# Optimization experiments

Measured on AMD Instinct MI355X. Metric: run time of the kernel, lower is better.

## Reference

```python
import jax, jax.numpy as jnp
import numpy as np

IN_DIM = 100000   # entity vocab
H_DIM = 128       # h_dim == dist_dim (forced in __init__)
K = 16            # num_neighbor
BOUNDARIES = jnp.array([1.0, 2.0, 4.0, 8.0, 16.0, 32.0, 64.0, 128.0], dtype=jnp.float32)
N_BUCKETS = BOUNDARIES.shape[0] + 1


def setup_inputs() -> dict:
    key = jax.random.key(0)
    ks = jax.random.split(key, 8)
    N = 100000
    node_ids = jax.random.randint(ks[0], (N,), 0, IN_DIM)
    nbr_idx = jax.random.randint(ks[1], (N, K), 0, N)
    nbr_dist = jax.random.uniform(ks[2], (N, K), dtype=jnp.float32) * 200.0
    scale = 1.0 / np.sqrt(H_DIM)
    embed_table = jax.random.normal(ks[3], (IN_DIM, H_DIM), dtype=jnp.float32) * scale
    dist_table = jax.random.normal(ks[4], (N_BUCKETS, H_DIM), dtype=jnp.float32) * scale
    W_self = jax.random.normal(ks[5], (H_DIM, H_DIM), dtype=jnp.float32) * scale
    W_nbr = jax.random.normal(ks[6], (H_DIM, H_DIM), dtype=jnp.float32) * scale
    b = jnp.zeros((H_DIM,), dtype=jnp.float32)
    return {
        "node_ids": node_ids, "nbr_idx": nbr_idx, "nbr_dist": nbr_dist,
        "embed_table": embed_table, "dist_table": dist_table,
        "W_self": W_self, "W_nbr": W_nbr, "b": b,
    }


def reference(node_ids, nbr_idx, nbr_dist, embed_table, dist_table, W_self, W_nbr, b):
    # h = self.embedding(h.squeeze())
    h = embed_table[node_ids]                       # [N, D] gather
    # DistRelConv: gather sampled neighbor features
    neigh = h[nbr_idx]                              # [N, K, D] gather
    # bucketize edge distances against boundaries -> distance-bucket embedding
    bucket = jnp.searchsorted(BOUNDARIES, nbr_dist) # [N, K] int
    msg = neigh + dist_table[bucket]                # [N, K, D]
    agg = jnp.mean(msg, axis=1)                     # [N, D]
    # merge='sum': self transform + neighbor transform, relu activation
    out = jax.nn.relu(h @ W_self + agg @ W_nbr + b) # [N, D]
    return out
```

## Files before the change

### kernel.cpp

```cpp
#include <hip/hip_runtime.h>
#include <stdint.h>

#define KNBR 16

typedef float f32x4 __attribute__((ext_vector_type(4)));
typedef float f32x2 __attribute__((ext_vector_type(2)));
typedef __bf16 bf16x8 __attribute__((ext_vector_type(8)));

union ABFrag { uint4 u; bf16x8 v; };

__device__ __forceinline__ uint32_t bf16_rne(float x) {
    uint32_t u = __float_as_uint(x);
    return (u + 0x7fffu + ((u >> 16) & 1u)) >> 16;
}

__device__ __forceinline__ uint32_t bucket_of(float d) {
    uint32_t u = __float_as_uint(d);
    int e = (int)((u >> 23) & 0xff) - 127;
    int b = e + ((u & 0x7fffffu) != 0 ? 1 : 0);
    return (uint32_t)min(max(b, 0), 8);
}

#define GLD(gsrc, ldst)                                                          \
    __builtin_amdgcn_global_load_lds(                                            \
        (const __attribute__((address_space(1))) void*)(gsrc),                   \
        (__attribute__((address_space(3))) void*)(ldst), 4, 0, 0)

__global__ void k_prep(const float* __restrict__ src, uint32_t* __restrict__ ebf,
                       uint32_t* __restrict__ e8, int n_dwords,
                       const float* __restrict__ Ws, const float* __restrict__ Wn,
                       uint16_t* __restrict__ Bp) {
    if (blockIdx.x < 2048) {
        int i = blockIdx.x * blockDim.x + threadIdx.x;
        int stride = 2048 * blockDim.x;
        for (; i < n_dwords; i += stride) {
            float4 v = ((const float4*)src)[i];
            ebf[2 * i]     = bf16_rne(v.x) | (bf16_rne(v.y) << 16);
            ebf[2 * i + 1] = bf16_rne(v.z) | (bf16_rne(v.w) << 16);
            uint32_t p = 0;
            p = __builtin_amdgcn_cvt_pk_fp8_f32(v.x, v.y, p, false);
            p = __builtin_amdgcn_cvt_pk_fp8_f32(v.z, v.w, p, true);
            e8[i] = p;
        }
    } else {
        int o = (blockIdx.x - 2048) * blockDim.x + threadIdx.x;
        if (o >= 8 * 8 * 64 * 8) return;
        int i = o & 7, lane = (o >> 3) & 63, nt = (o >> 9) & 7, ks = o >> 12;
        int r = ks * 32 + (lane >> 4) * 8 + i;
        int c = nt * 16 + (lane & 15);
        float v = (r < 128) ? Ws[r * 128 + c] : Wn[(r - 128) * 128 + c];
        Bp[o] = (uint16_t)bf16_rne(v);
    }
}

__global__ __launch_bounds__(256, 5) void k_fused(
    const int* __restrict__ node_ids, const int* __restrict__ nbr_idx,
    const float* __restrict__ nbr_dist,
    const uint32_t* __restrict__ emb_bf, const uint16_t* __restrict__ emb8,
    const float* __restrict__ dist_table, const float* __restrict__ bias,
    const uint32_t* __restrict__ Bp, float* __restrict__ out, int nht)
{
    __shared__ uint32_t L[4 * 2048];

    const int lane = threadIdx.x & 63;
    const int w = threadIdx.x >> 6;
    const int l_hi = lane >> 4;
    const int l_lo = lane & 15;
    uint32_t* Aw = L + w * 2048;
    uint32_t* Sw = Aw + 1024;
    float* Fw = (float*)Aw;

    const int ht = blockIdx.x * 4 + w;
    if (ht >= nht) return;

    f32x2 dreg[9];
    #pragma unroll
    for (int b = 0; b < 9; ++b) {
        float2 t = *(const float2*)(dist_table + b * 128 + 2 * lane);
        dreg[b] = (f32x2){t.x, t.y};
    }
    float breg[8];
    #pragma unroll
    for (int nt = 0; nt < 8; ++nt) breg[nt] = bias[nt * 16 + l_lo];

    int2 nb = *(const int2*)(nbr_idx + (size_t)ht * 128 + lane * 2);
    float2 dd = *(const float2*)(nbr_dist + (size_t)ht * 128 + lane * 2);
    uint32_t ea[2];
    ea[0] = ((uint32_t)node_ids[nb.x] & 0xFFFFFFu) | (bucket_of(dd.x) << 24);
    ea[1] = ((uint32_t)node_ids[nb.y] & 0xFFFFFFu) | (bucket_of(dd.y) << 24);
    uint32_t selfv = (uint32_t)node_ids[(size_t)ht * 8 + (lane & 7)];


#define ISSUE(J) do {                                                                     \
        const int sw_ = ((J) & 7) << 2;                                                   \
        const uint32_t sid_ = (uint32_t)__builtin_amdgcn_readlane((int)selfv, (J));       \
        GLD(emb_bf + (size_t)sid_ * 64 + (lane ^ sw_), Aw + (J) * 128);                   \
        uint32_t* sb_ = Sw + ((J) & 1) * 512;                                             \
        _Pragma("unroll")                                                                 \
        for (int m = 0; m < 8; ++m) {                                                     \
            const int L_ = 8 * (J) + m;                                                   \
            const uint32_t s0_ = (uint32_t)__builtin_amdgcn_readlane((int)ea[0], L_) & 0xFFFFFFu; \
            const uint32_t s1_ = (uint32_t)__builtin_amdgcn_readlane((int)ea[1], L_) & 0xFFFFFFu; \
            const uint32_t sel_ = (lane < 32) ? s0_ : s1_;                                \
            GLD((const uint8_t*)emb8 + (size_t)sel_ * 128 + (lane & 31) * 4, sb_ + m * 64); \
        }                                                                                 \
    } while (0)

#define CONSUME(J, VM) do {                                                               \
        asm volatile("s_waitcnt vmcnt(" #VM ")" ::: "memory");                            \
        const uint16_t* st_ = (const uint16_t*)(Sw + ((J) & 1) * 512);                    \
        f32x2 s_ = (f32x2){0.f, 0.f};                                                     \
        uint64_t c_ = 0;                                                                  \
        _Pragma("unroll")                                                                 \
        for (int k = 0; k < KNBR; ++k) {                                                  \
            const uint32_t ew_ = (uint32_t)__builtin_amdgcn_readlane((int)ea[k & 1], 8 * (J) + (k >> 1)); \
            c_ += 1ull << (5 * (ew_ >> 24));                                              \
            const uint32_t pv_ = (uint32_t)st_[k * 64 + lane];                            \
            s_ += __builtin_amdgcn_cvt_pk_f32_fp8(pv_, false);                            \
        }                                                                                 \
        _Pragma("unroll")                                                                 \
        for (int b = 0; b < 9; ++b) {                                                     \
            const float fb_ = (float)(uint32_t)((c_ >> (5 * b)) & 31u);                   \
            s_ += (f32x2){fb_, fb_} * dreg[b];                                            \
        }                                                                                 \
        s_ *= 0.0625f;                                                                    \
        const int sw_ = ((J) & 7) << 2;                                                   \
        Aw[(J) * 128 + (64 + (lane ^ sw_))] = bf16_rne(s_.x) | (bf16_rne(s_.y) << 16);    \
        __builtin_amdgcn_sched_barrier(0);                                                \
    } while (0)

    ISSUE(0); ISSUE(1);
    CONSUME(0, 9);  ISSUE(2);
    CONSUME(1, 9);  ISSUE(3);
    CONSUME(2, 9);  ISSUE(4);
    CONSUME(3, 9);  ISSUE(5);
    CONSUME(4, 9);  ISSUE(6);
    CONSUME(5, 9);  ISSUE(7);
    CONSUME(6, 9);
    CONSUME(7, 0);
#undef ISSUE
#undef CONSUME

    asm volatile("s_waitcnt vmcnt(0) lgkmcnt(0)" ::: "memory");
    __builtin_amdgcn_sched_barrier(0);

    f32x4 acc[8];
    #pragma unroll
    for (int t = 0; t < 8; ++t) acc[t] = (f32x4){0.f, 0.f, 0.f, 0.f};
    #pragma unroll
    for (int ks = 0; ks < 8; ++ks) {
        ABFrag a;
        a.u = *(const uint4*)(Aw + l_lo * 128 + ((ks * 16 + l_hi * 4) ^ ((l_lo & 7) << 2)));
        #pragma unroll
        for (int nt = 0; nt < 8; ++nt) {
            ABFrag b;
            b.u = ((const uint4*)Bp)[(ks * 8 + nt) * 64 + lane];
            acc[nt] = __builtin_amdgcn_mfma_f32_16x16x32_bf16(a.v, b.v, acc[nt], 0, 0, 0);
        }
    }

    #pragma unroll
    for (int nt = 0; nt < 8; ++nt) {
        const int col = nt * 16 + l_lo;
        #pragma unroll
        for (int r = 0; r < 4; ++r) {
            const int row = l_hi * 4 + r;
            if (row < 8) {
                float v = acc[nt][r] + breg[nt];
                Fw[row * 128 + (col ^ ((row & 7) << 2))] = v > 0.f ? v : 0.f;
            }
        }
    }
    float* dst = out + (size_t)ht * 1024;
    #pragma unroll
    for (int it = 0; it < 4; ++it) {
        const int f = it * 256 + lane * 4;
        const int r = f >> 7, c = f & 127;
        float4 v = *(const float4*)(Fw + r * 128 + (c ^ ((r & 7) << 2)));
        *(float4*)(dst + f) = v;
    }
}

__global__ void k_naive(const int* __restrict__ node_ids, const int* __restrict__ nbr_idx,
                        const float* __restrict__ nbr_dist, const float* __restrict__ emb,
                        const float* __restrict__ dt, const float* __restrict__ Ws,
                        const float* __restrict__ Wn, const float* __restrict__ bias,
                        float* __restrict__ out, int base) {
    __shared__ float h[128], ag[128];
    const int nd = base + blockIdx.x;
    const int t = threadIdx.x;
    const int nid = node_ids[nd];
    float hv = emb[(size_t)nid * 128 + t];
    float a = 0.f;
    for (int k = 0; k < KNBR; ++k) {
        int sn = node_ids[nbr_idx[(size_t)nd * KNBR + k]];
        int bkt = (int)bucket_of(nbr_dist[(size_t)nd * KNBR + k]);
        a += emb[(size_t)sn * 128 + t] + dt[bkt * 128 + t];
    }
    h[t] = hv; ag[t] = a * 0.0625f;
    __syncthreads();
    float s = bias[t];
    for (int d = 0; d < 128; ++d) s += h[d] * Ws[d * 128 + t] + ag[d] * Wn[d * 128 + t];
    out[(size_t)nd * 128 + t] = s > 0.f ? s : 0.f;
}

extern "C" void kernel_launch(void* const* d_in, const int* in_sizes, int n_in,
                              void* d_out, int out_size, void* d_ws, size_t ws_size,
                              hipStream_t stream) {
    const int* node_ids   = (const int*)d_in[0];
    const int* nbr_idx    = (const int*)d_in[1];
    const float* nbr_dist = (const float*)d_in[2];
    const float* emb      = (const float*)d_in[3];
    const float* dist_tab = (const float*)d_in[4];
    const float* Ws       = (const float*)d_in[5];
    const float* Wn       = (const float*)d_in[6];
    const float* bias     = (const float*)d_in[7];
    float* out = (float*)d_out;
    const int n = in_sizes[0];
    const int in_dim = in_sizes[3] / 128;

    const size_t offEbf = 65536;
    const size_t offE8  = offEbf + (size_t)in_dim * 256;
    const size_t needT  = offE8 + (size_t)in_dim * 128;

    if (ws_size < needT) {
        if (n > 0)
            k_naive<<<n, 128, 0, stream>>>(node_ids, nbr_idx, nbr_dist, emb, dist_tab, Ws, Wn, bias, out, 0);
        return;
    }
    uint16_t* Bp   = (uint16_t*)d_ws;
    uint32_t* ebf  = (uint32_t*)((char*)d_ws + offEbf);
    uint32_t* e8   = (uint32_t*)((char*)d_ws + offE8);

    k_prep<<<2176, 256, 0, stream>>>(emb, ebf, e8, in_dim * 32, Ws, Wn, Bp);

    const int nht = n >> 3;
    const int rem = n & 7;

    if (nht > 0) {
        const int nblocks = (nht + 3) >> 2;
        k_fused<<<nblocks, 256, 0, stream>>>(node_ids, nbr_idx, nbr_dist, ebf, (const uint16_t*)e8,
                                             dist_tab, bias, (const uint32_t*)Bp, out, nht);
    }
    if (rem > 0)
        k_naive<<<rem, 128, 0, stream>>>(node_ids, nbr_idx, nbr_dist, emb, dist_tab, Ws, Wn, bias, out, nht << 3);
}
```

Baseline: 82.76 us.

## Process two 8-node tiles per wave, overlapping next tile's gathers with MFMA

Each wave now handles two consecutive 8-node tiles. It prefetches the second tile's neighbor indices and distances while consuming the first, then issues the second tile's first gathers before running the first tile's MFMA and epilogue. The aim is to hide gather latency behind matrix math and the output store. In exchange, LDS per wave rises by half, launch bounds drop from 5 to 3, and the grid shrinks to half as many blocks, which lowers occupancy and parallelism.

```diff
diff --git a/kernel.cpp b/kernel.cpp
--- a/kernel.cpp
+++ b/kernel.cpp
@@ -53,25 +53,29 @@
     }
 }
 
-__global__ __launch_bounds__(256, 5) void k_fused(
+__global__ __launch_bounds__(256, 3) void k_fused(
     const int* __restrict__ node_ids, const int* __restrict__ nbr_idx,
     const float* __restrict__ nbr_dist,
     const uint32_t* __restrict__ emb_bf, const uint16_t* __restrict__ emb8,
     const float* __restrict__ dist_table, const float* __restrict__ bias,
     const uint32_t* __restrict__ Bp, float* __restrict__ out, int nht)
 {
-    __shared__ uint32_t L[4 * 2048];
+    __shared__ uint32_t L[4 * 3072];
 
     const int lane = threadIdx.x & 63;
     const int w = threadIdx.x >> 6;
     const int l_hi = lane >> 4;
     const int l_lo = lane & 15;
-    uint32_t* Aw = L + w * 2048;
-    uint32_t* Sw = Aw + 1024;
-    float* Fw = (float*)Aw;
-
-    const int ht = blockIdx.x * 4 + w;
-    if (ht >= nht) return;
+    uint32_t* const wbase = L + w * 3072;
+    uint32_t* const A0 = wbase;
+    uint32_t* const A1 = wbase + 1024;
+    uint32_t* const Sw = wbase + 2048;
+
+    const int wid = blockIdx.x * 4 + w;
+    const int ht0 = wid * 2;
+    if (ht0 >= nht) return;
+    const bool has1 = (ht0 + 1 < nht);
+    const int ht1c = min(ht0 + 1, nht - 1);
 
     f32x2 dreg[9];
     #pragma unroll
@@ -83,37 +87,37 @@
     #pragma unroll
     for (int nt = 0; nt < 8; ++nt) breg[nt] = bias[nt * 16 + l_lo];
 
-    int2 nb = *(const int2*)(nbr_idx + (size_t)ht * 128 + lane * 2);
-    float2 dd = *(const float2*)(nbr_dist + (size_t)ht * 128 + lane * 2);
-    uint32_t ea[2];
-    ea[0] = ((uint32_t)node_ids[nb.x] & 0xFFFFFFu) | (bucket_of(dd.x) << 24);
-    ea[1] = ((uint32_t)node_ids[nb.y] & 0xFFFFFFu) | (bucket_of(dd.y) << 24);
-    uint32_t selfv = (uint32_t)node_ids[(size_t)ht * 8 + (lane & 7)];
-
-
-#define ISSUE(J) do {                                                                     \
+    int2 nb = *(const int2*)(nbr_idx + (size_t)ht0 * 128 + lane * 2);
+    float2 dd = *(const float2*)(nbr_dist + (size_t)ht0 * 128 + lane * 2);
+    uint32_t selfv = (uint32_t)node_ids[(size_t)ht0 * 8 + (lane & 7)];
+    uint32_t ea0 = ((uint32_t)node_ids[nb.x] & 0xFFFFFFu) | (bucket_of(dd.x) << 24);
+    uint32_t ea1 = ((uint32_t)node_ids[nb.y] & 0xFFFFFFu) | (bucket_of(dd.y) << 24);
+
+
+#define ISSUE(J, AW) do {                                                                 \
         const int sw_ = ((J) & 7) << 2;                                                   \
         const uint32_t sid_ = (uint32_t)__builtin_amdgcn_readlane((int)selfv, (J));       \
-        GLD(emb_bf + (size_t)sid_ * 64 + (lane ^ sw_), Aw + (J) * 128);                   \
+        GLD(emb_bf + (size_t)sid_ * 64 + (lane ^ sw_), (AW) + (J) * 128);                 \
         uint32_t* sb_ = Sw + ((J) & 1) * 512;                                             \
         _Pragma("unroll")                                                                 \
         for (int m = 0; m < 8; ++m) {                                                     \
             const int L_ = 8 * (J) + m;                                                   \
-            const uint32_t s0_ = (uint32_t)__builtin_amdgcn_readlane((int)ea[0], L_) & 0xFFFFFFu; \
-            const uint32_t s1_ = (uint32_t)__builtin_amdgcn_readlane((int)ea[1], L_) & 0xFFFFFFu; \
+            const uint32_t s0_ = (uint32_t)__builtin_amdgcn_readlane((int)ea0, L_) & 0xFFFFFFu; \
+            const uint32_t s1_ = (uint32_t)__builtin_amdgcn_readlane((int)ea1, L_) & 0xFFFFFFu; \
             const uint32_t sel_ = (lane < 32) ? s0_ : s1_;                                \
             GLD((const uint8_t*)emb8 + (size_t)sel_ * 128 + (lane & 31) * 4, sb_ + m * 64); \
         }                                                                                 \
     } while (0)
 
-#define CONSUME(J, VM) do {                                                               \
+#define CONSUME(J, VM, AW) do {                                                           \
         asm volatile("s_waitcnt vmcnt(" #VM ")" ::: "memory");                            \
         const uint16_t* st_ = (const uint16_t*)(Sw + ((J) & 1) * 512);                    \
         f32x2 s_ = (f32x2){0.f, 0.f};                                                     \
         uint64_t c_ = 0;                                                                  \
         _Pragma("unroll")                                                                 \
         for (int k = 0; k < KNBR; ++k) {                                                  \
-            const uint32_t ew_ = (uint32_t)__builtin_amdgcn_readlane((int)ea[k & 1], 8 * (J) + (k >> 1)); \
+            const uint32_t ew_ = (uint32_t)__builtin_amdgcn_readlane(                     \
+                (int)((k & 1) ? ea1 : ea0), 8 * (J) + (k >> 1));                          \
             c_ += 1ull << (5 * (ew_ >> 24));                                              \
             const uint32_t pv_ = (uint32_t)st_[k * 64 + lane];                            \
             s_ += __builtin_amdgcn_cvt_pk_f32_fp8(pv_, false);                            \
@@ -125,60 +129,100 @@
         }                                                                                 \
         s_ *= 0.0625f;                                                                    \
         const int sw_ = ((J) & 7) << 2;                                                   \
-        Aw[(J) * 128 + (64 + (lane ^ sw_))] = bf16_rne(s_.x) | (bf16_rne(s_.y) << 16);    \
+        (AW)[(J) * 128 + (64 + (lane ^ sw_))] = bf16_rne(s_.x) | (bf16_rne(s_.y) << 16);  \
         __builtin_amdgcn_sched_barrier(0);                                                \
     } while (0)
 
-    ISSUE(0); ISSUE(1);
-    CONSUME(0, 9);  ISSUE(2);
-    CONSUME(1, 9);  ISSUE(3);
-    CONSUME(2, 9);  ISSUE(4);
-    CONSUME(3, 9);  ISSUE(5);
-    CONSUME(4, 9);  ISSUE(6);
-    CONSUME(5, 9);  ISSUE(7);
-    CONSUME(6, 9);
-    CONSUME(7, 0);
+#define MFMA_EPI(AW, HT) do {                                                             \
+        f32x4 acc[8];                                                                     \
+        _Pragma("unroll")                                                                 \
+        for (int t = 0; t < 8; ++t) acc[t] = (f32x4){0.f, 0.f, 0.f, 0.f};                 \
+        _Pragma("unroll")                                                                 \
+        for (int ks = 0; ks < 8; ++ks) {                                                  \
+            ABFrag a;                                                                     \
+            a.u = *(const uint4*)((AW) + l_lo * 128 + ((ks * 16 + l_hi * 4) ^ ((l_lo & 7) << 2))); \
+            _Pragma("unroll")                                                             \
+            for (int nt = 0; nt < 8; ++nt) {                                              \
+                ABFrag b;                                                                 \
+                b.u = ((const uint4*)Bp)[(ks * 8 + nt) * 64 + lane];                      \
+                acc[nt] = __builtin_amdgcn_mfma_f32_16x16x32_bf16(a.v, b.v, acc[nt], 0, 0, 0); \
+            }                                                                             \
+        }                                                                                 \
+        ISSUE_NEXT_HOOK;                                                                  \
+        float* Fw_ = (float*)(AW);                                                       \
+        _Pragma("unroll")                                                                 \
+        for (int nt = 0; nt < 8; ++nt) {                                                  \
+            const int col = nt * 16 + l_lo;                                               \
+            _Pragma("unroll")                                                             \
+            for (int r = 0; r < 4; ++r) {                                                 \
+                const int row = l_hi * 4 + r;                                             \
+                if (row < 8) {                                                            \
+                    float v = acc[nt][r] + breg[nt];                                      \
+                    Fw_[row * 128 + (col ^ ((row & 7) << 2))] = v > 0.f ? v : 0.f;        \
+                }                                                                         \
+            }                                                                             \
+        }                                                                                 \
+        float* dst_ = out + (size_t)(HT) * 1024;                                          \
+        _Pragma("unroll")                                                                 \
+        for (int it = 0; it < 4; ++it) {                                                  \
+            const int f = it * 256 + lane * 4;                                            \
+            const int r = f >> 7, c = f & 127;                                            \
+            float4 v = *(const float4*)(Fw_ + r * 128 + (c ^ ((r & 7) << 2)));            \
+            *(float4*)(dst_ + f) = v;                                                     \
+        }                                                                                 \
+    } while (0)
+
+    ISSUE(0, A0); ISSUE(1, A0);
+
+    CONSUME(0, 9, A0);  ISSUE(2, A0);
+    CONSUME(1, 9, A0);
+    int2 nb2 = *(const int2*)(nbr_idx + (size_t)ht1c * 128 + lane * 2);
+    float2 dd2 = *(const float2*)(nbr_dist + (size_t)ht1c * 128 + lane * 2);
+    uint32_t sv2 = (uint32_t)node_ids[(size_t)ht1c * 8 + (lane & 7)];
+    __builtin_amdgcn_sched_barrier(0);
+    ISSUE(3, A0);
+    CONSUME(2, 12, A0); ISSUE(4, A0);
+    CONSUME(3, 9, A0);  ISSUE(5, A0);
+    CONSUME(4, 9, A0);  ISSUE(6, A0);
+    int nid2x = node_ids[nb2.x];
+    int nid2y = node_ids[nb2.y];
+    __builtin_amdgcn_sched_barrier(0);
+    CONSUME(5, 11, A0); ISSUE(7, A0);
+    CONSUME(6, 11, A0);
+    CONSUME(7, 0, A0);
+
+    const uint32_t ean0 = ((uint32_t)nid2x & 0xFFFFFFu) | (bucket_of(dd2.x) << 24);
+    const uint32_t ean1 = ((uint32_t)nid2y & 0xFFFFFFu) | (bucket_of(dd2.y) << 24);
+
+    asm volatile("s_waitcnt lgkmcnt(0)" ::: "memory");
+    __builtin_amdgcn_sched_barrier(0);
+
+    ea0 = ean0; ea1 = ean1; selfv = sv2;
+#define ISSUE_NEXT_HOOK do { if (has1) { ISSUE(0, A1); ISSUE(1, A1); } } while (0)
+    MFMA_EPI(A0, ht0);
+#undef ISSUE_NEXT_HOOK
+
+    if (!has1) return;
+
+    CONSUME(0, 9, A1);  ISSUE(2, A1);
+    CONSUME(1, 9, A1);  ISSUE(3, A1);
+    CONSUME(2, 9, A1);  ISSUE(4, A1);
+    CONSUME(3, 9, A1);  ISSUE(5, A1);
+    CONSUME(4, 9, A1);  ISSUE(6, A1);
+    CONSUME(5, 9, A1);  ISSUE(7, A1);
+    CONSUME(6, 9, A1);
+    CONSUME(7, 0, A1);
+
+    asm volatile("s_waitcnt lgkmcnt(0)" ::: "memory");
+    __builtin_amdgcn_sched_barrier(0);
+
+#define ISSUE_NEXT_HOOK do { } while (0)
+    MFMA_EPI(A1, ht0 + 1);
+#undef ISSUE_NEXT_HOOK
+
 #undef ISSUE
 #undef CONSUME
-
-    asm volatile("s_waitcnt vmcnt(0) lgkmcnt(0)" ::: "memory");
-    __builtin_amdgcn_sched_barrier(0);
-
-    f32x4 acc[8];
-    #pragma unroll
-    for (int t = 0; t < 8; ++t) acc[t] = (f32x4){0.f, 0.f, 0.f, 0.f};
-    #pragma unroll
-    for (int ks = 0; ks < 8; ++ks) {
-        ABFrag a;
-        a.u = *(const uint4*)(Aw + l_lo * 128 + ((ks * 16 + l_hi * 4) ^ ((l_lo & 7) << 2)));
-        #pragma unroll
-        for (int nt = 0; nt < 8; ++nt) {
-            ABFrag b;
-            b.u = ((const uint4*)Bp)[(ks * 8 + nt) * 64 + lane];
-            acc[nt] = __builtin_amdgcn_mfma_f32_16x16x32_bf16(a.v, b.v, acc[nt], 0, 0, 0);
-        }
-    }
-
-    #pragma unroll
-    for (int nt = 0; nt < 8; ++nt) {
-        const int col = nt * 16 + l_lo;
-        #pragma unroll
-        for (int r = 0; r < 4; ++r) {
-            const int row = l_hi * 4 + r;
-            if (row < 8) {
-                float v = acc[nt][r] + breg[nt];
-                Fw[row * 128 + (col ^ ((row & 7) << 2))] = v > 0.f ? v : 0.f;
-            }
-        }
-    }
-    float* dst = out + (size_t)ht * 1024;
-    #pragma unroll
-    for (int it = 0; it < 4; ++it) {
-        const int f = it * 256 + lane * 4;
-        const int r = f >> 7, c = f & 127;
-        float4 v = *(const float4*)(Fw + r * 128 + (c ^ ((r & 7) << 2)));
-        *(float4*)(dst + f) = v;
-    }
+#undef MFMA_EPI
 }
 
 __global__ void k_naive(const int* __restrict__ node_ids, const int* __restrict__ nbr_idx,
@@ -238,7 +282,7 @@
     const int rem = n & 7;
 
     if (nht > 0) {
-        const int nblocks = (nht + 3) >> 2;
+        const int nblocks = (nht + 7) >> 3;
         k_fused<<<nblocks, 256, 0, stream>>>(node_ids, nbr_idx, nbr_dist, ebf, (const uint16_t*)e8,
                                              dist_tab, bias, (const uint32_t*)Bp, out, nht);
     }
```

After: 144.7 us. 74.9% more time.
